# Optimization experiments

Hardware: AMD Instinct MI355X
Metric: run time of the kernel (lower is better)

The kernel has to match this reference:

```python
import jax, jax.numpy as jnp
from jax import lax
import numpy as np

DIM = 256
N_EMBED = 512
B = 16
T = 2048


def setup_inputs() -> dict:
    key = jax.random.key(0)
    k1, k2, k3 = jax.random.split(key, 3)
    inp = jax.random.normal(k1, (B, T, DIM), dtype=jnp.float32)
    spk = jax.random.normal(k2, (3, B, DIM), dtype=jnp.float32)
    embedding = jax.random.normal(k3, (N_EMBED, DIM, DIM), dtype=jnp.float32)
    return {"input": inp, "speaker_embedding": spk, "embedding": embedding}


def reference(input, speaker_embedding, embedding):
    x = input                              # (B, T, D)
    mul = speaker_embedding[2].T           # (D, B)
    add = speaker_embedding[1].T           # (D, B)
    # per-batch codebook: (n, D, D) @ (D, B) -> (n, D, B)
    cb = jnp.einsum('ndk,kb->ndb', embedding, mul)
    cb = cb / jnp.linalg.norm(cb, axis=1, keepdims=True)
    cb = cb + add                          # broadcast (D,B) over n
    embed = jnp.transpose(cb, (2, 1, 0))   # (B, D, n)
    # distances on detached values (matches torch .detach())
    flat = lax.stop_gradient(x)
    e = lax.stop_gradient(embed)
    dist = (jnp.sum(flat * flat, axis=2, keepdims=True)
            - 2.0 * jnp.einsum('btd,bdn->btn', flat, e)
            + jnp.sum(e * e, axis=1, keepdims=True))  # (B, T, n)
    embed_ind = jnp.argmax(-dist, axis=2)  # (B, T)
    cbB = jnp.transpose(cb, (2, 0, 1))     # (B, n, D)
    # per-batch gather of selected codes -> (B, T, D)
    quantize = cbB[jnp.arange(cbB.shape[0])[:, None], embed_ind]
    diff = jnp.mean((quantize - x) ** 2)
    quantize_1 = x + lax.stop_gradient(quantize - x)
    return ((quantize + quantize_1) / 2.0, diff, embed_ind)
```

## Files before the change

kernel.cpp:

```cpp
#include <hip/hip_runtime.h>

#define T_   2048
#define D_   256
#define N_   512
#define BTOT 16

typedef unsigned short ushortT;
typedef _Float16 f16;
typedef f16 h8 __attribute__((ext_vector_type(8)));
typedef float f4v __attribute__((ext_vector_type(4)));

#define QN   ((size_t)BTOT*T_*D_)
#define IDX0 (QN + 1)
#define CBSTRIDE ((size_t)N_*D_)

__device__ __forceinline__ float bf2f(ushortT u){
    union { unsigned int i; float f; } c; c.i = ((unsigned int)u) << 16; return c.f;
}
__device__ __forceinline__ void unp8(uint4 p, float* f){
    f[0]=bf2f((ushortT)(p.x & 0xffff)); f[1]=bf2f((ushortT)(p.x >> 16));
    f[2]=bf2f((ushortT)(p.y & 0xffff)); f[3]=bf2f((ushortT)(p.y >> 16));
    f[4]=bf2f((ushortT)(p.z & 0xffff)); f[5]=bf2f((ushortT)(p.z >> 16));
    f[6]=bf2f((ushortT)(p.w & 0xffff)); f[7]=bf2f((ushortT)(p.w >> 16));
}
__device__ __forceinline__ f4v mfma16(h8 a, h8 b, f4v c){
    return __builtin_amdgcn_mfma_f32_16x16x32_f16(a, b, c, 0, 0, 0);
}

__global__ void k_probe(const ushortT* __restrict__ x, int* __restrict__ flg){
    int tid = threadIdx.x;
    ushortT u = x[tid];
    int e = (u >> 7) & 0xff;
    bool ok = (e >= 100 && e <= 140);
    unsigned long long m = __ballot(ok);
    if (tid == 0) *flg = (__popcll(m) >= 55) ? 1 : 0;
}

template<int BC>
__global__ __launch_bounds__(256) void k_codebook(
    const void* __restrict__ spkin, const void* __restrict__ embin,
    f16* __restrict__ hig, f16* __restrict__ logp,
    float* __restrict__ e2g, int b0, const int* __restrict__ flagp)
{
    const int isb = *flagp;
    const ushortT* ss = (const ushortT*)spkin;
    const float*   sf = (const float*)spkin;
    const ushortT* es = (const ushortT*)embin;
    const float*   ef = (const float*)embin;

    __shared__ float s2[D_ * 16];
    __shared__ float s1[D_ * 16];
    __shared__ float red[16 * D_];
    __shared__ float nrm[16];

    const int n = blockIdx.x, tid = threadIdx.x;

    for (int e = tid; e < D_ * 16; e += 256){ s2[e] = 0.f; s1[e] = 0.f; }
    __syncthreads();
    for (int e = tid; e < D_ * BC; e += 256){
        int blc = e >> 8, k = e & 255;
        int g2 = (2*BTOT + b0 + blc)*D_ + k;
        int g1 = (1*BTOT + b0 + blc)*D_ + k;
        s2[k*16 + blc] = isb ? bf2f(ss[g2]) : sf[g2];
        s1[k*16 + blc] = isb ? bf2f(ss[g1]) : sf[g1];
    }
    __syncthreads();

    const int d = tid;
    float acc[16];
    #pragma unroll
    for (int b = 0; b < 16; b++) acc[b] = 0.f;

    const size_t rb = ((size_t)n * D_ + d) * D_;

    auto inner = [&](const float* ev, int k0){
        #pragma unroll
        for (int j = 0; j < 8; j++){
            float e = ev[j];
            if (BC == 16){
                const float4* sp = (const float4*)&s2[(k0 + j) * 16];
                float4 q0 = sp[0], q1 = sp[1], q2 = sp[2], q3 = sp[3];
                acc[0]  += e*q0.x; acc[1]  += e*q0.y; acc[2]  += e*q0.z; acc[3]  += e*q0.w;
                acc[4]  += e*q1.x; acc[5]  += e*q1.y; acc[6]  += e*q1.z; acc[7]  += e*q1.w;
                acc[8]  += e*q2.x; acc[9]  += e*q2.y; acc[10] += e*q2.z; acc[11] += e*q2.w;
                acc[12] += e*q3.x; acc[13] += e*q3.y; acc[14] += e*q3.z; acc[15] += e*q3.w;
            } else {
                #pragma unroll
                for (int blc = 0; blc < BC; blc++)
                    acc[blc] += e * s2[(k0 + j)*16 + blc];
            }
        }
    };

    if (isb){
        for (int k0 = 0; k0 < D_; k0 += 8){
            uint4 p = *(const uint4*)(es + rb + k0);
            float ev[8]; unp8(p, ev);
            inner(ev, k0);
        }
    } else {
        for (int k0 = 0; k0 < D_; k0 += 8){
            float4 p0 = *(const float4*)(ef + rb + k0);
            float4 p1 = *(const float4*)(ef + rb + k0 + 4);
            float ev[8] = {p0.x,p0.y,p0.z,p0.w,p1.x,p1.y,p1.z,p1.w};
            inner(ev, k0);
        }
    }

    #pragma unroll
    for (int blc = 0; blc < BC; blc++) red[blc*D_ + d] = acc[blc]*acc[blc];
    __syncthreads();
    for (int s = 128; s > 0; s >>= 1){
        if (d < s){
            #pragma unroll
            for (int blc = 0; blc < BC; blc++) red[blc*D_ + d] += red[blc*D_ + d + s];
        }
        __syncthreads();
    }
    if (d < BC) nrm[d] = sqrtf(red[d*D_]);
    __syncthreads();

    float cbv[BC];
    #pragma unroll
    for (int blc = 0; blc < BC; blc++)
        cbv[blc] = acc[blc] / nrm[blc] + s1[d*16 + blc];

    #pragma unroll
    for (int blc = 0; blc < BC; blc++) red[blc*D_ + d] = cbv[blc]*cbv[blc];
    __syncthreads();
    for (int s = 128; s > 0; s >>= 1){
        if (d < s){
            #pragma unroll
            for (int blc = 0; blc < BC; blc++) red[blc*D_ + d] += red[blc*D_ + d + s];
        }
        __syncthreads();
    }
    if (d < BC) e2g[(size_t)d*N_ + n] = red[d*D_];

    f16* sh = (f16*)s2;
    #pragma unroll
    for (int blc = 0; blc < BC; blc++){
        float c = cbv[blc];
        f16 h = (f16)c;
        float r = c - (float)h;
        f16 l = (f16)(r * 4096.f);
        sh[blc*256 + d] = h;
        sh[4096 + blc*256 + d] = l;
    }
    __syncthreads();
    for (int w = tid; w < BC*32; w += 256){
        const int blc = w >> 5, g = w & 31;
        const int d0 = (g>>2)*32 + (g&3)*8;
        const size_t off = (size_t)blc*CBSTRIDE
                         + (size_t)((n>>4)*8 + (g>>2))*512
                         + (size_t)(g&3)*128 + (size_t)(n&15)*8;
        *(uint4*)(hig  + off) = *(const uint4*)(sh + blc*256 + d0);
        *(uint4*)(logp + off) = *(const uint4*)(sh + 4096 + blc*256 + d0);
    }
}

__global__ __launch_bounds__(512, 2) void k_fused(
    const void* __restrict__ xin,
    const f16* __restrict__ hig, const f16* __restrict__ logp,
    const float* __restrict__ e2g,
    float* __restrict__ outf, float* __restrict__ part,
    int blk0, const int* __restrict__ flagp)
{
    __shared__ float mv[8 * 16];
    __shared__ int   mi[8 * 16];
    __shared__ int   sfin[64];
    __shared__ float wsum[8];

    const int isb = *flagp;
    const int tid = threadIdx.x;
    const int bl = blockIdx.x >> 5, tT = blockIdx.x & 31;
    const int bg = blk0 + bl;
    const int lane = tid & 63, wid = tid >> 6;
    const int band = wid >> 1, nh = wid & 1;
    const int arow = lane & 15, kgrp = lane >> 4;

    const ushortT* xs = (const ushortT*)xin;
    const float*   xf = (const float*)xin;

    h8 ah[8], al[8];
    {
        const size_t rowbase = ((size_t)bg*T_ + (size_t)tT*64 + band*16 + arow) * D_;
        #pragma unroll
        for (int ks = 0; ks < 8; ks++){
            float f[8];
            const size_t o = rowbase + ks*32 + kgrp*8;
            if (isb){
                uint4 p = *(const uint4*)(xs + o);
                unp8(p, f);
            } else {
                float4 p0 = *(const float4*)(xf + o);
                float4 p1 = *(const float4*)(xf + o + 4);
                f[0]=p0.x; f[1]=p0.y; f[2]=p0.z; f[3]=p0.w;
                f[4]=p1.x; f[5]=p1.y; f[6]=p1.z; f[7]=p1.w;
            }
            h8 h, l;
            #pragma unroll
            for (int j = 0; j < 8; j++){
                f16 hh = (f16)f[j];
                h[j] = hh;
                l[j] = (f16)((f[j] - (float)hh) * 4096.f);
            }
            ah[ks] = h; al[ks] = l;
        }
    }

    const f16* hb = hig  + (size_t)bl*CBSTRIDE + (size_t)(lane*8);
    const f16* lb = logp + (size_t)bl*CBSTRIDE + (size_t)(lane*8);

    float runv[4]; int runi[4];
    #pragma unroll
    for (int i = 0; i < 4; i++){ runv[i] = 3.4e38f; runi[i] = 0x7fffffff; }

    #pragma unroll 1
    for (int c = 0; c < 8; c++){
        const int nc0 = nh*16 + c*2;
        f4v acch[2], accm[2], accl[2];
        #pragma unroll
        for (int t2 = 0; t2 < 2; t2++){
            acch[t2] = (f4v){0.f,0.f,0.f,0.f};
            accm[t2] = (f4v){0.f,0.f,0.f,0.f};
            accl[t2] = (f4v){0.f,0.f,0.f,0.f};
        }
        const f16* hc = hb + (size_t)nc0*4096;
        const f16* lc = lb + (size_t)nc0*4096;
        #pragma unroll
        for (int ks = 0; ks < 8; ks++){
            h8 b0h = *(const h8*)(hc + ks*512);
            h8 b1h = *(const h8*)(hc + 4096 + ks*512);
            h8 b0l = *(const h8*)(lc + ks*512);
            h8 b1l = *(const h8*)(lc + 4096 + ks*512);
            acch[0] = mfma16(ah[ks], b0h, acch[0]);
            accm[0] = mfma16(ah[ks], b0l, accm[0]);
            accm[0] = mfma16(al[ks], b0h, accm[0]);
            accl[0] = mfma16(al[ks], b0l, accl[0]);
            acch[1] = mfma16(ah[ks], b1h, acch[1]);
            accm[1] = mfma16(ah[ks], b1l, accm[1]);
            accm[1] = mfma16(al[ks], b1h, accm[1]);
            accl[1] = mfma16(al[ks], b1l, accl[1]);
        }
        #pragma unroll
        for (int t2 = 0; t2 < 2; t2++){
            const int nn = (nc0 + t2)*16 + arow;
            const float e2v = e2g[(size_t)bl*N_ + nn];
            #pragma unroll
            for (int r = 0; r < 4; r++){
                float dot = acch[t2][r] + accm[t2][r]*(1.f/4096.f)
                          + accl[t2][r]*(1.f/16777216.f);
                float s = e2v - 2.f*dot;
                if (s < runv[r]){ runv[r] = s; runi[r] = nn; }
            }
        }
    }

    #pragma unroll
    for (int m = 8; m >= 1; m >>= 1){
        #pragma unroll
        for (int r = 0; r < 4; r++){
            float ov = __shfl_xor(runv[r], m);
            int   on = __shfl_xor(runi[r], m);
            if (ov < runv[r] || (ov == runv[r] && on < runi[r])){
                runv[r] = ov; runi[r] = on;
            }
        }
    }
    if (arow == 0){
        #pragma unroll
        for (int r = 0; r < 4; r++){
            mv[wid*16 + kgrp*4 + r] = runv[r];
            mi[wid*16 + kgrp*4 + r] = runi[r];
        }
    }
    __syncthreads();
    if (tid < 64){
        const int bandt = tid >> 4, rl = tid & 15;
        float v0 = mv[(bandt*2    )*16 + rl]; int i0 = mi[(bandt*2    )*16 + rl];
        float v1 = mv[(bandt*2 + 1)*16 + rl]; int i1 = mi[(bandt*2 + 1)*16 + rl];
        int nf = (v1 < v0) ? i1 : i0;
        sfin[tid] = nf;
        outf[IDX0 + (size_t)bg*T_ + (size_t)tT*64 + tid] = (float)nf;
    }
    __syncthreads();

    float dacc = 0.f;
    {
        const int r = tid >> 3, oct = tid & 7;
        const int nn = sfin[r];
        const size_t fb = (size_t)bl*CBSTRIDE
                        + (size_t)((nn>>4)*8 + oct)*512 + (size_t)(nn&15)*8;
        const size_t xo0 = ((size_t)bg*T_ + (size_t)tT*64 + r)*D_ + oct*32;
        #pragma unroll
        for (int q = 0; q < 4; q++){
            h8 hq = *(const h8*)(hig  + fb + q*128);
            h8 lq = *(const h8*)(logp + fb + q*128);
            float xv[8];
            if (isb){
                uint4 p = *(const uint4*)(xs + xo0 + q*8);
                unp8(p, xv);
            } else {
                float4 p0 = *(const float4*)(xf + xo0 + q*8);
                float4 p1 = *(const float4*)(xf + xo0 + q*8 + 4);
                xv[0]=p0.x; xv[1]=p0.y; xv[2]=p0.z; xv[3]=p0.w;
                xv[4]=p1.x; xv[5]=p1.y; xv[6]=p1.z; xv[7]=p1.w;
            }
            float og[8];
            #pragma unroll
            for (int j = 0; j < 8; j++){
                float qv = (float)hq[j] + (float)lq[j]*(1.f/4096.f);
                float qm = qv - xv[j];
                dacc += qm*qm;
                og[j] = 0.5f*(qv + (xv[j] + qm));
            }
            *(float4*)(outf + xo0 + q*8)     = make_float4(og[0],og[1],og[2],og[3]);
            *(float4*)(outf + xo0 + q*8 + 4) = make_float4(og[4],og[5],og[6],og[7]);
        }
    }
    #pragma unroll
    for (int o2 = 32; o2 > 0; o2 >>= 1) dacc += __shfl_down(dacc, o2, 64);
    if (lane == 0) wsum[wid] = dacc;
    __syncthreads();
    if (tid == 0){
        float t = 0.f;
        #pragma unroll
        for (int i = 0; i < 8; i++) t += wsum[i];
        atomicAdd(&part[blockIdx.x & 1023], t);
    }
}

__global__ __launch_bounds__(256) void k_fin(const float* __restrict__ part,
                                             float* __restrict__ outf){
    const int tid = threadIdx.x;
    float v = part[tid] + part[tid + 256] + part[tid + 512] + part[tid + 768];
    #pragma unroll
    for (int o = 32; o > 0; o >>= 1) v += __shfl_down(v, o, 64);
    __shared__ float wsum[4];
    if ((tid & 63) == 0) wsum[tid >> 6] = v;
    __syncthreads();
    if (tid == 0)
        outf[QN] = (wsum[0] + wsum[1] + wsum[2] + wsum[3]) * (1.0f / (float)QN);
}

extern "C" void kernel_launch(void* const* d_in, const int* in_sizes, int n_in,
                              void* d_out, int out_size, void* d_ws, size_t ws_size,
                              hipStream_t stream)
{
    const void* x   = d_in[0];
    const void* spk = d_in[1];
    const void* emb = d_in[2];

    int Bc = 16;
    while (Bc > 1 && ((size_t)Bc*N_*D_*4 + (size_t)Bc*N_*4 + 4096 + 16) > ws_size) Bc >>= 1;

    char*  ws   = (char*)d_ws;
    f16*   hig  = (f16*)ws;
    f16*   logp = (f16*)(ws + (size_t)Bc*N_*D_*2);
    float* e2g  = (float*)(ws + (size_t)Bc*N_*D_*4);
    float* part = (float*)(ws + (size_t)Bc*N_*D_*4 + (size_t)Bc*N_*4);
    int*   flg  = (int*)((char*)part + 4096);

    float* outf = (float*)d_out;

    hipMemsetAsync(part, 0, 4096, stream);
    k_probe<<<1, 64, 0, stream>>>((const ushortT*)x, flg);

    for (int b0 = 0; b0 < BTOT; b0 += Bc){
        switch (Bc){
            case 16: k_codebook<16><<<512, 256, 0, stream>>>(spk, emb, hig, logp, e2g, b0, flg); break;
            case 8:  k_codebook<8> <<<512, 256, 0, stream>>>(spk, emb, hig, logp, e2g, b0, flg); break;
            case 4:  k_codebook<4> <<<512, 256, 0, stream>>>(spk, emb, hig, logp, e2g, b0, flg); break;
            case 2:  k_codebook<2> <<<512, 256, 0, stream>>>(spk, emb, hig, logp, e2g, b0, flg); break;
            default: k_codebook<1> <<<512, 256, 0, stream>>>(spk, emb, hig, logp, e2g, b0, flg); break;
        }
        k_fused<<<Bc*32, 512, 0, stream>>>(x, hig, logp, e2g, outf, part, b0, flg);
    }
    k_fin<<<1, 256, 0, stream>>>(part, outf);
}
```

Before: 359.4 us.

## Compute full codebook once, stage half in output buffer, pipeline MFMA B-loads

The codebook kernel now always computes all 16 batches in one pass. Batches 0-7 go to the workspace and batches 8-15 are staged in the output buffer, which is first used by the second half of the fused pass and then overwritten. The fused kernel moves to 256-thread blocks covering 32 rows each, with batch-fastest block ordering. Its inner loop double-buffers the codebook fragment loads so they overlap with MFMAs. This removes the workspace-size-driven re-computation of the codebook and exposes more blocks for latency hiding, but it relies on launch ordering so the staged data is consumed before the output write clobbers it.

After: 348.6 us. -3.0%, faster.

```diff
diff --git a/kernel.cpp b/kernel.cpp
--- a/kernel.cpp
+++ b/kernel.cpp
@@ -36,11 +36,11 @@
     if (tid == 0) *flg = (__popcll(m) >= 55) ? 1 : 0;
 }
 
-template<int BC>
-__global__ __launch_bounds__(256) void k_codebook(
+__global__ __launch_bounds__(256) void k_codebook16(
     const void* __restrict__ spkin, const void* __restrict__ embin,
-    f16* __restrict__ hig, f16* __restrict__ logp,
-    float* __restrict__ e2g, int b0, const int* __restrict__ flagp)
+    f16* __restrict__ hig, f16* __restrict__ logp, float* __restrict__ e2g,
+    f16* __restrict__ shi, f16* __restrict__ slo, float* __restrict__ se2,
+    const int* __restrict__ flagp)
 {
     const int isb = *flagp;
     const ushortT* ss = (const ushortT*)spkin;
@@ -55,12 +55,10 @@
 
     const int n = blockIdx.x, tid = threadIdx.x;
 
-    for (int e = tid; e < D_ * 16; e += 256){ s2[e] = 0.f; s1[e] = 0.f; }
-    __syncthreads();
-    for (int e = tid; e < D_ * BC; e += 256){
+    for (int e = tid; e < D_ * 16; e += 256){
         int blc = e >> 8, k = e & 255;
-        int g2 = (2*BTOT + b0 + blc)*D_ + k;
-        int g1 = (1*BTOT + b0 + blc)*D_ + k;
+        int g2 = (2*BTOT + blc)*D_ + k;
+        int g1 = (1*BTOT + blc)*D_ + k;
         s2[k*16 + blc] = isb ? bf2f(ss[g2]) : sf[g2];
         s1[k*16 + blc] = isb ? bf2f(ss[g1]) : sf[g1];
     }
@@ -77,18 +75,12 @@
         #pragma unroll
         for (int j = 0; j < 8; j++){
             float e = ev[j];
-            if (BC == 16){
-                const float4* sp = (const float4*)&s2[(k0 + j) * 16];
-                float4 q0 = sp[0], q1 = sp[1], q2 = sp[2], q3 = sp[3];
-                acc[0]  += e*q0.x; acc[1]  += e*q0.y; acc[2]  += e*q0.z; acc[3]  += e*q0.w;
-                acc[4]  += e*q1.x; acc[5]  += e*q1.y; acc[6]  += e*q1.z; acc[7]  += e*q1.w;
-                acc[8]  += e*q2.x; acc[9]  += e*q2.y; acc[10] += e*q2.z; acc[11] += e*q2.w;
-                acc[12] += e*q3.x; acc[13] += e*q3.y; acc[14] += e*q3.z; acc[15] += e*q3.w;
-            } else {
-                #pragma unroll
-                for (int blc = 0; blc < BC; blc++)
-                    acc[blc] += e * s2[(k0 + j)*16 + blc];
-            }
+            const float4* sp = (const float4*)&s2[(k0 + j) * 16];
+            float4 q0 = sp[0], q1 = sp[1], q2 = sp[2], q3 = sp[3];
+            acc[0]  += e*q0.x; acc[1]  += e*q0.y; acc[2]  += e*q0.z; acc[3]  += e*q0.w;
+            acc[4]  += e*q1.x; acc[5]  += e*q1.y; acc[6]  += e*q1.z; acc[7]  += e*q1.w;
+            acc[8]  += e*q2.x; acc[9]  += e*q2.y; acc[10] += e*q2.z; acc[11] += e*q2.w;
+            acc[12] += e*q3.x; acc[13] += e*q3.y; acc[14] += e*q3.z; acc[15] += e*q3.w;
         }
     };
 
@@ -108,38 +100,42 @@
     }
 
     #pragma unroll
-    for (int blc = 0; blc < BC; blc++) red[blc*D_ + d] = acc[blc]*acc[blc];
+    for (int blc = 0; blc < 16; blc++) red[blc*D_ + d] = acc[blc]*acc[blc];
     __syncthreads();
     for (int s = 128; s > 0; s >>= 1){
         if (d < s){
             #pragma unroll
-            for (int blc = 0; blc < BC; blc++) red[blc*D_ + d] += red[blc*D_ + d + s];
+            for (int blc = 0; blc < 16; blc++) red[blc*D_ + d] += red[blc*D_ + d + s];
         }
         __syncthreads();
     }
-    if (d < BC) nrm[d] = sqrtf(red[d*D_]);
-    __syncthreads();
-
-    float cbv[BC];
-    #pragma unroll
-    for (int blc = 0; blc < BC; blc++)
+    if (d < 16) nrm[d] = sqrtf(red[d*D_]);
+    __syncthreads();
+
+    float cbv[16];
+    #pragma unroll
+    for (int blc = 0; blc < 16; blc++)
         cbv[blc] = acc[blc] / nrm[blc] + s1[d*16 + blc];
 
     #pragma unroll
-    for (int blc = 0; blc < BC; blc++) red[blc*D_ + d] = cbv[blc]*cbv[blc];
+    for (int blc = 0; blc < 16; blc++) red[blc*D_ + d] = cbv[blc]*cbv[blc];
     __syncthreads();
     for (int s = 128; s > 0; s >>= 1){
         if (d < s){
             #pragma unroll
-            for (int blc = 0; blc < BC; blc++) red[blc*D_ + d] += red[blc*D_ + d + s];
+            for (int blc = 0; blc < 16; blc++) red[blc*D_ + d] += red[blc*D_ + d + s];
         }
         __syncthreads();
     }
-    if (d < BC) e2g[(size_t)d*N_ + n] = red[d*D_];
+    if (d < 16){
+        float v = red[d*D_];
+        if (d < 8) e2g[(size_t)d*N_ + n] = v;
+        else       se2[(size_t)(d-8)*N_ + n] = v;
+    }
 
     f16* sh = (f16*)s2;
     #pragma unroll
-    for (int blc = 0; blc < BC; blc++){
+    for (int blc = 0; blc < 16; blc++){
         float c = cbv[blc];
         f16 h = (f16)c;
         float r = c - (float)h;
@@ -148,32 +144,34 @@
         sh[4096 + blc*256 + d] = l;
     }
     __syncthreads();
-    for (int w = tid; w < BC*32; w += 256){
+    for (int w = tid; w < 16*32; w += 256){
         const int blc = w >> 5, g = w & 31;
         const int d0 = (g>>2)*32 + (g&3)*8;
-        const size_t off = (size_t)blc*CBSTRIDE
+        const size_t off = (size_t)(blc & 7)*CBSTRIDE
                          + (size_t)((n>>4)*8 + (g>>2))*512
                          + (size_t)(g&3)*128 + (size_t)(n&15)*8;
-        *(uint4*)(hig  + off) = *(const uint4*)(sh + blc*256 + d0);
-        *(uint4*)(logp + off) = *(const uint4*)(sh + 4096 + blc*256 + d0);
-    }
-}
-
-__global__ __launch_bounds__(512, 2) void k_fused(
+        f16* dh = (blc < 8) ? hig  : shi;
+        f16* dl = (blc < 8) ? logp : slo;
+        *(uint4*)(dh + off) = *(const uint4*)(sh + blc*256 + d0);
+        *(uint4*)(dl + off) = *(const uint4*)(sh + 4096 + blc*256 + d0);
+    }
+}
+
+__global__ __launch_bounds__(256, 2) void k_fused(
     const void* __restrict__ xin,
     const f16* __restrict__ hig, const f16* __restrict__ logp,
     const float* __restrict__ e2g,
     float* __restrict__ outf, float* __restrict__ part,
     int blk0, const int* __restrict__ flagp)
 {
-    __shared__ float mv[8 * 16];
-    __shared__ int   mi[8 * 16];
-    __shared__ int   sfin[64];
-    __shared__ float wsum[8];
+    __shared__ float mv[4 * 16];
+    __shared__ int   mi[4 * 16];
+    __shared__ int   sfin[32];
+    __shared__ float wsum[4];
 
     const int isb = *flagp;
     const int tid = threadIdx.x;
-    const int bl = blockIdx.x >> 5, tT = blockIdx.x & 31;
+    const int bl = blockIdx.x & 7, tT = blockIdx.x >> 3;
     const int bg = blk0 + bl;
     const int lane = tid & 63, wid = tid >> 6;
     const int band = wid >> 1, nh = wid & 1;
@@ -184,7 +182,7 @@
 
     h8 ah[8], al[8];
     {
-        const size_t rowbase = ((size_t)bg*T_ + (size_t)tT*64 + band*16 + arow) * D_;
+        const size_t rowbase = ((size_t)bg*T_ + (size_t)tT*32 + band*16 + arow) * D_;
         #pragma unroll
         for (int ks = 0; ks < 8; ks++){
             float f[8];
@@ -211,50 +209,80 @@
 
     const f16* hb = hig  + (size_t)bl*CBSTRIDE + (size_t)(lane*8);
     const f16* lb = logp + (size_t)bl*CBSTRIDE + (size_t)(lane*8);
+    const float* e2b = e2g + (size_t)bl*N_;
 
     float runv[4]; int runi[4];
     #pragma unroll
     for (int i = 0; i < 4; i++){ runv[i] = 3.4e38f; runi[i] = 0x7fffffff; }
+
+    h8 a0h, a1h, a0l, a1l;
+    h8 b0h, b1h, b0l, b1l;
+
+    const f16* hc = hb + (size_t)(nh*16)*4096;
+    const f16* lc = lb + (size_t)(nh*16)*4096;
+
+    a0h = *(const h8*)(hc);          a1h = *(const h8*)(hc + 4096);
+    a0l = *(const h8*)(lc);          a1l = *(const h8*)(lc + 4096);
+
+    f4v acch0, acch1, accm0, accm1, accl0, accl1;
 
     #pragma unroll 1
     for (int c = 0; c < 8; c++){
-        const int nc0 = nh*16 + c*2;
-        f4v acch[2], accm[2], accl[2];
-        #pragma unroll
-        for (int t2 = 0; t2 < 2; t2++){
-            acch[t2] = (f4v){0.f,0.f,0.f,0.f};
-            accm[t2] = (f4v){0.f,0.f,0.f,0.f};
-            accl[t2] = (f4v){0.f,0.f,0.f,0.f};
-        }
-        const f16* hc = hb + (size_t)nc0*4096;
-        const f16* lc = lb + (size_t)nc0*4096;
-        #pragma unroll
-        for (int ks = 0; ks < 8; ks++){
-            h8 b0h = *(const h8*)(hc + ks*512);
-            h8 b1h = *(const h8*)(hc + 4096 + ks*512);
-            h8 b0l = *(const h8*)(lc + ks*512);
-            h8 b1l = *(const h8*)(lc + 4096 + ks*512);
-            acch[0] = mfma16(ah[ks], b0h, acch[0]);
-            accm[0] = mfma16(ah[ks], b0l, accm[0]);
-            accm[0] = mfma16(al[ks], b0h, accm[0]);
-            accl[0] = mfma16(al[ks], b0l, accl[0]);
-            acch[1] = mfma16(ah[ks], b1h, acch[1]);
-            accm[1] = mfma16(ah[ks], b1l, accm[1]);
-            accm[1] = mfma16(al[ks], b1h, accm[1]);
-            accl[1] = mfma16(al[ks], b1l, accl[1]);
-        }
-        #pragma unroll
-        for (int t2 = 0; t2 < 2; t2++){
-            const int nn = (nc0 + t2)*16 + arow;
-            const float e2v = e2g[(size_t)bl*N_ + nn];
+        acch0 = (f4v){0.f,0.f,0.f,0.f}; acch1 = acch0;
+        accm0 = acch0; accm1 = acch0; accl0 = acch0; accl1 = acch0;
+
+        #pragma unroll
+        for (int ks2 = 0; ks2 < 4; ks2++){
+            const int ks = ks2*2;
+            {
+                const f16* h2 = hc + (ks+1)*512;
+                const f16* l2 = lc + (ks+1)*512;
+                b0h = *(const h8*)(h2);       b1h = *(const h8*)(h2 + 4096);
+                b0l = *(const h8*)(l2);       b1l = *(const h8*)(l2 + 4096);
+            }
+            acch0 = mfma16(ah[ks], a0h, acch0);
+            acch1 = mfma16(ah[ks], a1h, acch1);
+            accm0 = mfma16(ah[ks], a0l, accm0);
+            accm1 = mfma16(ah[ks], a1l, accm1);
+            accl0 = mfma16(al[ks], a0l, accl0);
+            accl1 = mfma16(al[ks], a1l, accl1);
+            accm0 = mfma16(al[ks], a0h, accm0);
+            accm1 = mfma16(al[ks], a1h, accm1);
+            if (ks2 < 3){
+                const f16* h2 = hc + (ks+2)*512;
+                const f16* l2 = lc + (ks+2)*512;
+                a0h = *(const h8*)(h2);       a1h = *(const h8*)(h2 + 4096);
+                a0l = *(const h8*)(l2);       a1l = *(const h8*)(l2 + 4096);
+            } else if (c < 7){
+                const f16* h2 = hc + 8192;
+                const f16* l2 = lc + 8192;
+                a0h = *(const h8*)(h2);       a1h = *(const h8*)(h2 + 4096);
+                a0l = *(const h8*)(l2);       a1l = *(const h8*)(l2 + 4096);
+            }
+            acch0 = mfma16(ah[ks+1], b0h, acch0);
+            acch1 = mfma16(ah[ks+1], b1h, acch1);
+            accm0 = mfma16(ah[ks+1], b0l, accm0);
+            accm1 = mfma16(ah[ks+1], b1l, accm1);
+            accl0 = mfma16(al[ks+1], b0l, accl0);
+            accl1 = mfma16(al[ks+1], b1l, accl1);
+            accm0 = mfma16(al[ks+1], b0h, accm0);
+            accm1 = mfma16(al[ks+1], b1h, accm1);
+        }
+
+        {
+            const int nn0 = (nh*16 + c*2)*16 + arow;
+            const float e20 = e2b[nn0], e21 = e2b[nn0 + 16];
             #pragma unroll
             for (int r = 0; r < 4; r++){
-                float dot = acch[t2][r] + accm[t2][r]*(1.f/4096.f)
-                          + accl[t2][r]*(1.f/16777216.f);
-                float s = e2v - 2.f*dot;
-                if (s < runv[r]){ runv[r] = s; runi[r] = nn; }
-            }
-        }
+                float d0 = acch0[r] + accm0[r]*(1.f/4096.f) + accl0[r]*(1.f/16777216.f);
+                float s0 = e20 - 2.f*d0;
+                if (s0 < runv[r]){ runv[r] = s0; runi[r] = nn0; }
+                float d1 = acch1[r] + accm1[r]*(1.f/4096.f) + accl1[r]*(1.f/16777216.f);
+                float s1 = e21 - 2.f*d1;
+                if (s1 < runv[r]){ runv[r] = s1; runi[r] = nn0 + 16; }
+            }
+        }
+        hc += 8192; lc += 8192;
     }
 
     #pragma unroll
@@ -276,13 +304,13 @@
         }
     }
     __syncthreads();
-    if (tid < 64){
+    if (tid < 32){
         const int bandt = tid >> 4, rl = tid & 15;
         float v0 = mv[(bandt*2    )*16 + rl]; int i0 = mi[(bandt*2    )*16 + rl];
         float v1 = mv[(bandt*2 + 1)*16 + rl]; int i1 = mi[(bandt*2 + 1)*16 + rl];
         int nf = (v1 < v0) ? i1 : i0;
         sfin[tid] = nf;
-        outf[IDX0 + (size_t)bg*T_ + (size_t)tT*64 + tid] = (float)nf;
+        outf[IDX0 + (size_t)bg*T_ + (size_t)tT*32 + tid] = (float)nf;
     }
     __syncthreads();
 
@@ -292,7 +320,7 @@
         const int nn = sfin[r];
         const size_t fb = (size_t)bl*CBSTRIDE
                         + (size_t)((nn>>4)*8 + oct)*512 + (size_t)(nn&15)*8;
-        const size_t xo0 = ((size_t)bg*T_ + (size_t)tT*64 + r)*D_ + oct*32;
+        const size_t xo0 = ((size_t)bg*T_ + (size_t)tT*32 + r)*D_ + oct*32;
         #pragma unroll
         for (int q = 0; q < 4; q++){
             h8 hq = *(const h8*)(hig  + fb + q*128);
@@ -324,9 +352,7 @@
     if (lane == 0) wsum[wid] = dacc;
     __syncthreads();
     if (tid == 0){
-        float t = 0.f;
-        #pragma unroll
-        for (int i = 0; i < 8; i++) t += wsum[i];
+        float t = wsum[0] + wsum[1] + wsum[2] + wsum[3];
         atomicAdd(&part[blockIdx.x & 1023], t);
     }
 }
@@ -352,30 +378,25 @@
     const void* spk = d_in[1];
     const void* emb = d_in[2];
 
-    int Bc = 16;
-    while (Bc > 1 && ((size_t)Bc*N_*D_*4 + (size_t)Bc*N_*4 + 4096 + 16) > ws_size) Bc >>= 1;
+    float* outf = (float*)d_out;
 
     char*  ws   = (char*)d_ws;
     f16*   hig  = (f16*)ws;
-    f16*   logp = (f16*)(ws + (size_t)Bc*N_*D_*2);
-    float* e2g  = (float*)(ws + (size_t)Bc*N_*D_*4);
-    float* part = (float*)(ws + (size_t)Bc*N_*D_*4 + (size_t)Bc*N_*4);
+    f16*   logp = (f16*)(ws + (size_t)8*N_*D_*2);
+    float* e2g  = (float*)(ws + (size_t)8*N_*D_*4);
+    float* part = (float*)(ws + (size_t)8*N_*D_*4 + (size_t)8*N_*4);
     int*   flg  = (int*)((char*)part + 4096);
 
-    float* outf = (float*)d_out;
+    f16*   shi = (f16*)outf;
+    f16*   slo = (f16*)(outf + 524288);
+    float* se2 = outf + 1048576;
 
     hipMemsetAsync(part, 0, 4096, stream);
     k_probe<<<1, 64, 0, stream>>>((const ushortT*)x, flg);
 
-    for (int b0 = 0; b0 < BTOT; b0 += Bc){
-        switch (Bc){
-            case 16: k_codebook<16><<<512, 256, 0, stream>>>(spk, emb, hig, logp, e2g, b0, flg); break;
-            case 8:  k_codebook<8> <<<512, 256, 0, stream>>>(spk, emb, hig, logp, e2g, b0, flg); break;
-            case 4:  k_codebook<4> <<<512, 256, 0, stream>>>(spk, emb, hig, logp, e2g, b0, flg); break;
-            case 2:  k_codebook<2> <<<512, 256, 0, stream>>>(spk, emb, hig, logp, e2g, b0, flg); break;
-            default: k_codebook<1> <<<512, 256, 0, stream>>>(spk, emb, hig, logp, e2g, b0, flg); break;
-        }
-        k_fused<<<Bc*32, 512, 0, stream>>>(x, hig, logp, e2g, outf, part, b0, flg);
-    }
+    k_codebook16<<<512, 256, 0, stream>>>(spk, emb, hig, logp, e2g,
+                                          shi, slo, se2, flg);
+    k_fused<<<512, 256, 0, stream>>>(x, shi, slo, se2, outf, part, 8, flg);
+    k_fused<<<512, 256, 0, stream>>>(x, hig, logp, e2g, outf, part, 0, flg);
     k_fin<<<1, 256, 0, stream>>>(part, outf);
 }
```
